# Optimization experiments

Hardware: AMD Instinct MI355X
Metric: run time of the kernel (lower is better)

The kernel has to match this reference:

```python
import jax, jax.numpy as jnp
import numpy as np
import math

B, L, H, E = 16, 512, 8, 64


def setup_inputs() -> dict:
    key = jax.random.key(0)
    k0, k1, k2, k3 = jax.random.split(key, 4)
    return {
        "queries": jax.random.normal(k0, (B, L, H, E), jnp.float32),
        "keys": jax.random.normal(k1, (B, L, H, E), jnp.float32),
        "values": jax.random.normal(k2, (B, L, H, E), jnp.float32),
        "sigma": jax.random.normal(k3, (B, L, H), jnp.float32),
        "attn_mask": jnp.zeros((B, L, L), dtype=bool),  # unused: mask_flag=False
    }


def reference(queries, keys, values, sigma, attn_mask):
    # queries/keys: [B,L,H,E], values: [B,S,H,D], sigma: [B,L,H]
    Edim = queries.shape[-1]
    scale = 1.0 / math.sqrt(Edim)
    scores = jnp.einsum("blhe,bshe->bhls", queries, keys)
    attn = scale * scores  # mask_flag=False -> no causal mask

    # learned sigma -> positive bandwidth in (1e-5, 2]
    sig = jnp.transpose(sigma, (0, 2, 1))  # [B,H,L]
    sig = jax.nn.sigmoid(sig * 5.0) + 1e-5
    sig = jnp.power(3.0, sig) - 1.0
    sig = sig[..., None]  # [B,H,L,1]

    win = attn.shape[-1]
    idx = jnp.arange(win)
    dist = jnp.abs(idx[:, None] - idx[None, :]).astype(attn.dtype)  # |i-j|, [L,L]
    inv_sqrt_2pi = 1.0 / math.sqrt(2.0 * math.pi)
    prior = inv_sqrt_2pi / sig * jnp.exp(-(dist ** 2) / (2.0 * sig ** 2))  # [B,H,L,L]

    series = jax.nn.softmax(attn, axis=-1)  # dropout p=0.0 -> identity
    V = jnp.einsum("bhls,bshd->blhd", series, values)
    sigma_full = jnp.broadcast_to(sig, prior.shape)
    # output_attention=True
    return V, series, prior, sigma_full
```

## Files before the change

kernel.cpp:

```cpp
#include <hip/hip_runtime.h>
#include <hip/hip_bf16.h>
#include <math.h>

#define B_ 16
#define L_ 512
#define H_ 8
#define E_ 64

typedef float f32x4 __attribute__((ext_vector_type(4)));
typedef short bf16x8 __attribute__((ext_vector_type(8)));
typedef short s16x4 __attribute__((ext_vector_type(4)));
typedef unsigned int u32x4 __attribute__((ext_vector_type(4)));

__device__ __forceinline__ short f2bf(float f) {
    __hip_bfloat16 h = __float2bfloat16(f);
    return __builtin_bit_cast(short, h);
}

__device__ __forceinline__ bf16x8 cvt8(const float* p) {
    f32x4 a = *(const f32x4*)p;
    f32x4 b = *(const f32x4*)(p + 4);
    bf16x8 r;
    r[0] = f2bf(a[0]); r[1] = f2bf(a[1]); r[2] = f2bf(a[2]); r[3] = f2bf(a[3]);
    r[4] = f2bf(b[0]); r[5] = f2bf(b[1]); r[6] = f2bf(b[2]); r[7] = f2bf(b[3]);
    return r;
}

__global__ void qk_prep(const float* __restrict__ Qg, const float* __restrict__ Kg,
                        unsigned short* __restrict__ Qf, unsigned short* __restrict__ Kf) {
    int bid = blockIdx.x;
    int tg = bid & 7, bh = (bid >> 3) & 127, sel = bid >> 10;
    const float* src = sel ? Kg : Qg;
    unsigned short* dst = sel ? Kf : Qf;
    int h = bh & 7, b = bh >> 3;
    int t = threadIdx.x;
    int w = t >> 6, l = t & 63, lm = l & 15, g = l >> 4;
    int tile = tg * 4 + w;
    int row = tile * 16 + lm;
    const float* p = src + ((size_t)(b * 512 + row) * 8 + h) * 64 + g * 8;
    unsigned short* d0 = dst + ((size_t)(bh * 32 + tile) * 2) * 512 + l * 8;
    bf16x8 v0 = cvt8(p);
    bf16x8 v1 = cvt8(p + 32);
    *(bf16x8*)d0        = v0;
    *(bf16x8*)(d0 + 512) = v1;
}

__global__ void v_prep(const float* __restrict__ V, unsigned short* __restrict__ Vtf) {
    __shared__ float tile[64][68];
    int bid = blockIdx.x;
    int sc = bid & 7, bh = bid >> 3;
    int h = bh & 7, b = bh >> 3;
    int t = threadIdx.x;
    const float* vb = V + ((size_t)(b * 512 + sc * 64) * 8 + h) * 64;
    #pragma unroll
    for (int i = 0; i < 4; ++i) {
        int srow = i * 16 + (t >> 4);
        int d4 = (t & 15) * 4;
        f32x4 v = *(const f32x4*)(vb + (size_t)srow * 512 + d4);
        tile[srow][d4 + 0] = v[0]; tile[srow][d4 + 1] = v[1];
        tile[srow][d4 + 2] = v[2]; tile[srow][d4 + 3] = v[3];
    }
    __syncthreads();
    int dt = t >> 6, l = t & 63, lm = l & 15, g = l >> 4;
    #pragma unroll
    for (int ksl = 0; ksl < 2; ++ksl) {
        int ks = sc * 2 + ksl;
        bf16x8 u;
        #pragma unroll
        for (int j = 0; j < 8; ++j)
            u[j] = f2bf(tile[ksl * 32 + g * 8 + j][dt * 16 + lm]);
        *(bf16x8*)(Vtf + ((size_t)(bh * 4 + dt) * 16 + ks) * 512 + l * 8) = u;
    }
}

__launch_bounds__(256, 2)
__global__ void attn_fused(const unsigned short* __restrict__ Qf,
                           const unsigned short* __restrict__ Kf,
                           const unsigned short* __restrict__ Vtf,
                           const float* __restrict__ sigma,
                           float* __restrict__ Vout,
                           float* __restrict__ series,
                           float* __restrict__ prior,
                           float* __restrict__ sigf) {
    __shared__ __align__(16) char lds[4 * 16384];
    int tid = threadIdx.x;
    int w = tid >> 6, l = tid & 63, lm = l & 15, g = l >> 4;

    int bid = blockIdx.x;
    int nid = (bid & 7) * 128 + (bid >> 3);
    int rb = nid & 7, bh = nid >> 3;
    int h = bh & 7, b = bh >> 3;
    int qt = rb * 4 + w;
    int l0 = qt * 16;

    char* wl = lds + w * 16384;
    int swz = (lm & 7) << 4;

    const unsigned short* qfp = Qf + ((size_t)(bh * 32 + qt) * 2) * 512 + l * 8;
    bf16x8 qf0 = *(const bf16x8*)qfp;
    bf16x8 qf1 = *(const bf16x8*)(qfp + 512);

    const unsigned short* kfp = Kf + (size_t)bh * 32768 + l * 8;
    f32x4 acc[32];
    #pragma unroll
    for (int t = 0; t < 32; ++t) acc[t] = 0.0f;
    #pragma unroll
    for (int t = 0; t < 32; ++t) {
        bf16x8 k0 = *(const bf16x8*)(kfp + t * 1024);
        bf16x8 k1 = *(const bf16x8*)(kfp + t * 1024 + 512);
        acc[t] = __builtin_amdgcn_mfma_f32_16x16x32_bf16(k0, qf0, acc[t], 0, 0, 0);
        acc[t] = __builtin_amdgcn_mfma_f32_16x16x32_bf16(k1, qf1, acc[t], 0, 0, 0);
    }

    float m = -1e30f;
    #pragma unroll
    for (int t = 0; t < 32; ++t)
        m = fmaxf(m, fmaxf(fmaxf(acc[t][0], acc[t][1]), fmaxf(acc[t][2], acc[t][3])));
    m = fmaxf(m, __shfl_xor(m, 16));
    m = fmaxf(m, __shfl_xor(m, 32));
    const float SC = 0.125f * 1.44269504088896340736f;
    float ssum = 0.0f;
    #pragma unroll
    for (int t = 0; t < 32; ++t) {
        f32x4 p;
        #pragma unroll
        for (int r = 0; r < 4; ++r) {
            p[r] = exp2f((acc[t][r] - m) * SC);
            ssum += p[r];
        }
        acc[t] = p;
    }
    ssum += __shfl_xor(ssum, 16);
    ssum += __shfl_xor(ssum, 32);
    float inv = 1.0f / ssum;

    float* sp = series + ((size_t)bh * 512 + l0 + lm) * 512 + g * 4;
    #pragma unroll
    for (int t = 0; t < 32; ++t) {
        f32x4 p = acc[t];
        s16x4 pw;
        pw[0] = f2bf(p[0]); pw[1] = f2bf(p[1]); pw[2] = f2bf(p[2]); pw[3] = f2bf(p[3]);
        *(s16x4*)(wl + (((lm << 10) + 32 * t + 8 * g) ^ swz)) = pw;
        f32x4 sv; sv[0] = p[0] * inv; sv[1] = p[1] * inv; sv[2] = p[2] * inv; sv[3] = p[3] * inv;
        *(f32x4*)(sp + t * 16) = sv;
    }

    f32x4 oacc[4];
    #pragma unroll
    for (int dt = 0; dt < 4; ++dt) oacc[dt] = 0.0f;
    const unsigned short* vfp = Vtf + (size_t)bh * 32768 + l * 8;
    #pragma unroll
    for (int ks = 0; ks < 16; ++ks) {
        bf16x8 pb = *(const bf16x8*)(wl + (((lm << 10) + 64 * ks + 16 * g) ^ swz));
        #pragma unroll
        for (int dt = 0; dt < 4; ++dt) {
            bf16x8 va = *(const bf16x8*)(vfp + (size_t)(dt * 16 + ks) * 512);
            oacc[dt] = __builtin_amdgcn_mfma_f32_16x16x32_bf16(va, pb, oacc[dt], 0, 0, 0);
        }
    }

    float* Olds = (float*)wl;
    #pragma unroll
    for (int dt = 0; dt < 4; ++dt)
        #pragma unroll
        for (int r = 0; r < 4; ++r)
            Olds[(dt * 16 + g * 4 + r) * 17 + lm] = oacc[dt][r] * inv;
    #pragma unroll
    for (int it = 0; it < 4; ++it) {
        int rr = it * 4 + g;
        f32x4 o;
        #pragma unroll
        for (int e = 0; e < 4; ++e) o[e] = Olds[(lm * 4 + e) * 17 + rr];
        *(f32x4*)(Vout + ((size_t)(b * 512 + l0 + rr) * 8 + h) * 64 + lm * 4) = o;
    }

    int row_l = l0 + lm;
    float x = sigma[((size_t)b * 512 + row_l) * 8 + h];
    float s = 1.0f / (1.0f + exp2f(-7.2134752044448170368f * x)) + 1e-5f;
    float sg = exp2f(1.5849625007211562f * s) - 1.0f;
    float invc = 0.3989422804014327f / sg;
    float c2 = -0.72134752044448170368f / (sg * sg);
    size_t pbase = ((size_t)bh * 512 + row_l) * 512 + g * 128;
    f32x4 sgv; sgv[0] = sg; sgv[1] = sg; sgv[2] = sg; sgv[3] = sg;
    #pragma unroll
    for (int c4 = 0; c4 < 32; ++c4) {
        int j0 = g * 128 + c4 * 4;
        f32x4 pr;
        #pragma unroll
        for (int k = 0; k < 4; ++k) {
            float d = (float)(row_l - (j0 + k));
            pr[k] = invc * exp2f(c2 * d * d);
        }
        *(f32x4*)(prior + pbase + c4 * 4) = pr;
        *(f32x4*)(sigf + pbase + c4 * 4) = sgv;
    }
}

extern "C" void kernel_launch(void* const* d_in, const int* in_sizes, int n_in,
                              void* d_out, int out_size, void* d_ws, size_t ws_size,
                              hipStream_t stream) {
    const float* queries = (const float*)d_in[0];
    const float* keys    = (const float*)d_in[1];
    const float* values  = (const float*)d_in[2];
    const float* sigma   = (const float*)d_in[3];

    float* out = (float*)d_out;
    const size_t nV = (size_t)B_ * L_ * H_ * E_;
    const size_t nS = (size_t)B_ * H_ * L_ * L_;
    float* Vout       = out;
    float* series     = out + nV;
    float* prior      = out + nV + nS;
    float* sigma_full = out + nV + 2 * nS;

    unsigned short* Qf  = (unsigned short*)d_ws;
    unsigned short* Kf  = Qf + nV;
    unsigned short* Vtf = Kf + nV;

    qk_prep<<<2048, 256, 0, stream>>>(queries, keys, Qf, Kf);
    v_prep<<<1024, 256, 0, stream>>>(values, Vtf);
    attn_fused<<<1024, 256, 0, stream>>>(Qf, Kf, Vtf, sigma,
                                         Vout, series, prior, sigma_full);
}
```

Baseline: 571.8 us.

## Split prior/sigma output into separate coalesced streaming kernel with precomputed sigma

Moves the Gaussian prior and broadcast sigma writes out of the attention kernel into a dedicated kernel where each wave writes whole rows contiguously. A small kernel precomputes the transformed sigma bandwidth into workspace. This lightens the attention kernel and makes the dominant output stores fully coalesced, at the cost of two extra launches. It also changes the v_prep LDS padding.

```diff
diff --git a/kernel.cpp b/kernel.cpp
--- a/kernel.cpp
+++ b/kernel.cpp
@@ -10,7 +10,6 @@
 typedef float f32x4 __attribute__((ext_vector_type(4)));
 typedef short bf16x8 __attribute__((ext_vector_type(8)));
 typedef short s16x4 __attribute__((ext_vector_type(4)));
-typedef unsigned int u32x4 __attribute__((ext_vector_type(4)));
 
 __device__ __forceinline__ short f2bf(float f) {
     __hip_bfloat16 h = __float2bfloat16(f);
@@ -26,6 +25,15 @@
     return r;
 }
 
+__global__ void sig_kernel(const float* __restrict__ sigma, float* __restrict__ sig_ws) {
+    int o = blockIdx.x * 256 + threadIdx.x;
+    int l = o & 511, bh = o >> 9;
+    int h = bh & 7, b = bh >> 3;
+    float x = sigma[((size_t)(b * 512 + l)) * 8 + h];
+    float s = 1.0f / (1.0f + exp2f(-7.2134752044448170368f * x)) + 1e-5f;
+    sig_ws[o] = exp2f(1.5849625007211562f * s) - 1.0f;
+}
+
 __global__ void qk_prep(const float* __restrict__ Qg, const float* __restrict__ Kg,
                         unsigned short* __restrict__ Qf, unsigned short* __restrict__ Kf) {
     int bid = blockIdx.x;
@@ -39,14 +47,12 @@
     int row = tile * 16 + lm;
     const float* p = src + ((size_t)(b * 512 + row) * 8 + h) * 64 + g * 8;
     unsigned short* d0 = dst + ((size_t)(bh * 32 + tile) * 2) * 512 + l * 8;
-    bf16x8 v0 = cvt8(p);
-    bf16x8 v1 = cvt8(p + 32);
-    *(bf16x8*)d0        = v0;
-    *(bf16x8*)(d0 + 512) = v1;
+    *(bf16x8*)d0         = cvt8(p);
+    *(bf16x8*)(d0 + 512) = cvt8(p + 32);
 }
 
 __global__ void v_prep(const float* __restrict__ V, unsigned short* __restrict__ Vtf) {
-    __shared__ float tile[64][68];
+    __shared__ float tile[64][67];
     int bid = blockIdx.x;
     int sc = bid & 7, bh = bid >> 3;
     int h = bh & 7, b = bh >> 3;
@@ -74,14 +80,11 @@
 }
 
 __launch_bounds__(256, 2)
-__global__ void attn_fused(const unsigned short* __restrict__ Qf,
-                           const unsigned short* __restrict__ Kf,
-                           const unsigned short* __restrict__ Vtf,
-                           const float* __restrict__ sigma,
-                           float* __restrict__ Vout,
-                           float* __restrict__ series,
-                           float* __restrict__ prior,
-                           float* __restrict__ sigf) {
+__global__ void attn_kernel(const unsigned short* __restrict__ Qf,
+                            const unsigned short* __restrict__ Kf,
+                            const unsigned short* __restrict__ Vtf,
+                            float* __restrict__ Vout,
+                            float* __restrict__ series) {
     __shared__ __align__(16) char lds[4 * 16384];
     int tid = threadIdx.x;
     int w = tid >> 6, l = tid & 63, lm = l & 15, g = l >> 4;
@@ -173,26 +176,36 @@
         for (int e = 0; e < 4; ++e) o[e] = Olds[(lm * 4 + e) * 17 + rr];
         *(f32x4*)(Vout + ((size_t)(b * 512 + l0 + rr) * 8 + h) * 64 + lm * 4) = o;
     }
-
-    int row_l = l0 + lm;
-    float x = sigma[((size_t)b * 512 + row_l) * 8 + h];
-    float s = 1.0f / (1.0f + exp2f(-7.2134752044448170368f * x)) + 1e-5f;
-    float sg = exp2f(1.5849625007211562f * s) - 1.0f;
-    float invc = 0.3989422804014327f / sg;
-    float c2 = -0.72134752044448170368f / (sg * sg);
-    size_t pbase = ((size_t)bh * 512 + row_l) * 512 + g * 128;
-    f32x4 sgv; sgv[0] = sg; sgv[1] = sg; sgv[2] = sg; sgv[3] = sg;
-    #pragma unroll
-    for (int c4 = 0; c4 < 32; ++c4) {
-        int j0 = g * 128 + c4 * 4;
-        f32x4 pr;
-        #pragma unroll
-        for (int k = 0; k < 4; ++k) {
-            float d = (float)(row_l - (j0 + k));
-            pr[k] = invc * exp2f(c2 * d * d);
+}
+
+__launch_bounds__(256)
+__global__ void prior_kernel2(const float* __restrict__ sig_ws,
+                              float* __restrict__ prior,
+                              float* __restrict__ sigf) {
+    int t = threadIdx.x;
+    int w = t >> 6, l = t & 63;
+    int row0 = blockIdx.x * 16 + w * 4;
+    #pragma unroll
+    for (int r = 0; r < 4; ++r) {
+        int row = row0 + r;
+        int row_l = row & 511;
+        float sg = sig_ws[row];
+        float invc = 0.3989422804014327f / sg;
+        float c2 = -0.72134752044448170368f / (sg * sg);
+        size_t base = (size_t)row * 512;
+        f32x4 sgv; sgv[0] = sg; sgv[1] = sg; sgv[2] = sg; sgv[3] = sg;
+        #pragma unroll
+        for (int j = 0; j < 2; ++j) {
+            int c0 = j * 256 + l * 4;
+            f32x4 pr;
+            #pragma unroll
+            for (int k = 0; k < 4; ++k) {
+                float d = (float)(row_l - (c0 + k));
+                pr[k] = invc * exp2f(c2 * d * d);
+            }
+            *(f32x4*)(prior + base + c0) = pr;
+            *(f32x4*)(sigf + base + c0) = sgv;
         }
-        *(f32x4*)(prior + pbase + c4 * 4) = pr;
-        *(f32x4*)(sigf + pbase + c4 * 4) = sgv;
     }
 }
 
@@ -215,9 +228,11 @@
     unsigned short* Qf  = (unsigned short*)d_ws;
     unsigned short* Kf  = Qf + nV;
     unsigned short* Vtf = Kf + nV;
-
+    float* sig_ws = (float*)(Vtf + nV);
+
+    sig_kernel<<<B_ * H_ * L_ / 256, 256, 0, stream>>>(sigma, sig_ws);
     qk_prep<<<2048, 256, 0, stream>>>(queries, keys, Qf, Kf);
     v_prep<<<1024, 256, 0, stream>>>(values, Vtf);
-    attn_fused<<<1024, 256, 0, stream>>>(Qf, Kf, Vtf, sigma,
-                                         Vout, series, prior, sigma_full);
-}
+    attn_kernel<<<1024, 256, 0, stream>>>(Qf, Kf, Vtf, Vout, series);
+    prior_kernel2<<<4096, 256, 0, stream>>>(sig_ws, prior, sigma_full);
+}
```

New measurement: 481.1 us. -15.8%, faster.
